# Kernel tuning notes

Hardware: AMD Instinct MI355X
Metric: run time of the kernel (lower is better)

The kernel has to match this reference:

```python
import jax, jax.numpy as jnp
import numpy as np

N_NODES = 100000
D = 256            # in_channels
H = 256            # hidden_channels
E = 1000000        # number of query pairs


def setup_inputs() -> dict:
    key = jax.random.key(0)
    ks = jax.random.split(key, 8)
    x = jax.random.normal(ks[0], (N_NODES, D), dtype=jnp.float32)
    edge_index = jax.random.randint(ks[1], (2, 1000), 0, N_NODES, dtype=jnp.int64)
    edge_pairs = jax.random.randint(ks[2], (E, 2), 0, N_NODES, dtype=jnp.int64)
    # MLP params (Linear stores y = x @ W + b, W shaped [in, out])
    s1 = 1.0 / np.sqrt(D)
    s2 = 1.0 / np.sqrt(H)
    s3 = 1.0 / np.sqrt(H // 2)
    W1 = jax.random.uniform(ks[3], (D, H), jnp.float32, -s1, s1)
    b1 = jnp.zeros((H,), jnp.float32)
    W2 = jax.random.uniform(ks[4], (H, H // 2), jnp.float32, -s2, s2)
    b2 = jnp.zeros((H // 2,), jnp.float32)
    W3 = jax.random.uniform(ks[5], (H // 2, 1), jnp.float32, -s3, s3)
    b3 = jnp.zeros((1,), jnp.float32)
    return {"x": x, "W1": W1, "b1": b1, "W2": W2, "b2": b2,
            "W3": W3, "b3": b3, "edge_index": edge_index, "edge_pairs": edge_pairs}


def reference(x, W1, b1, W2, b2, W3, b3, edge_index, edge_pairs):
    # Gather node pairs and form elementwise-product pair features [E, D]
    feats = x[edge_pairs[:, 0]] * x[edge_pairs[:, 1]]
    # 3-layer MLP (dropout inactive at inference)
    h = jax.nn.relu(feats @ W1 + b1)
    h = jax.nn.relu(h @ W2 + b2)
    scores = h @ W3 + b3
    return scores.reshape(-1)
```

## Files before the change

### kernel.cpp

```cpp
#include <hip/hip_runtime.h>


typedef __attribute__((ext_vector_type(8))) short short8;
typedef __attribute__((ext_vector_type(4))) float floatx4;
typedef __attribute__((ext_vector_type(4))) unsigned uintx4;
typedef __attribute__((ext_vector_type(2))) int intx2;

#define MT 64
#define NTHREADS 1024
#define NBLOCKS 512

__device__ __forceinline__ unsigned short f2bf(float f) {
  union { float f; unsigned u; } a; a.f = f;
  unsigned r = a.u + 0x7FFFu + ((a.u >> 16) & 1u);
  return (unsigned short)(r >> 16);
}

__device__ __forceinline__ unsigned bf16mul2(unsigned ua, unsigned ub) {
  float lo = __uint_as_float(ua << 16)          * __uint_as_float(ub << 16);
  float hi = __uint_as_float(ua & 0xFFFF0000u) * __uint_as_float(ub & 0xFFFF0000u);
  return (unsigned)f2bf(lo) | ((unsigned)f2bf(hi) << 16);
}

__global__ void cast_x_kernel(const float* __restrict__ x, unsigned short* __restrict__ xb, int n4) {
  int i = blockIdx.x * blockDim.x + threadIdx.x;
  if (i >= n4) return;
  float4 v = ((const float4*)x)[i];
  ushort4 o;
  o.x = f2bf(v.x); o.y = f2bf(v.y); o.z = f2bf(v.z); o.w = f2bf(v.w);
  ((ushort4*)xb)[i] = o;
}

__global__ void prep_w_kernel(const float* __restrict__ W1, const float* __restrict__ W2,
                              unsigned short* __restrict__ w1t, unsigned short* __restrict__ w2t) {
  int i = blockIdx.x * blockDim.x + threadIdx.x;
  if (i < 256 * 256) {
    int k = i >> 8, n = i & 255;
    w1t[n * 256 + k] = f2bf(W1[k * 256 + n]);
  } else {
    int j = i - 256 * 256;
    if (j < 128 * 256) {
      int k = j >> 7, n = j & 127;
      w2t[n * 256 + k] = f2bf(W2[k * 128 + n]);
    }
  }
}

__global__ void init_out_kernel(float* __restrict__ out, const float* __restrict__ b3, int E) {
  int i = blockIdx.x * blockDim.x + threadIdx.x;
  if (i < E) out[i] = b3[0];
}

__global__ __launch_bounds__(NTHREADS, 4) void mlp_kernel(
    const unsigned short* __restrict__ xb,
    const unsigned short* __restrict__ w1t,
    const unsigned short* __restrict__ w2t,
    const float* __restrict__ b1,
    const float* __restrict__ b2,
    const float* __restrict__ w3,
    const int* __restrict__ ep,
    float* __restrict__ out,
    int E)
{
  __shared__ __align__(16) unsigned short buf[2][MT * 256];

  const int tid  = threadIdx.x;
  const int wv   = tid >> 6;
  const int lane = tid & 63;
  const int q    = lane >> 4;
  const int r16  = lane & 15;
  const int c    = tid & 31;
  const int mr0  = tid >> 5;

  const int ntiles = (E + MT - 1) / MT;

  {
    int t0 = blockIdx.x;
    #pragma unroll
    for (int s = 0; s < 2; ++s) {
      int m = mr0 + 32 * s;
      int g = t0 * MT + m; if (g >= E) g = E - 1;
      intx2 uv = __builtin_nontemporal_load((const intx2*)(ep + 2 * (size_t)g));
      uintx4 a = __builtin_nontemporal_load((const uintx4*)(xb + ((size_t)uv.x << 8) + (c << 3)));
      uintx4 b = __builtin_nontemporal_load((const uintx4*)(xb + ((size_t)uv.y << 8) + (c << 3)));
      uintx4 pv;
      #pragma unroll
      for (int tt = 0; tt < 4; ++tt) pv[tt] = bf16mul2(a[tt], b[tt]);
      *(uintx4*)((char*)buf[0] + m * 512 + ((c ^ (m & 15)) << 4)) = pv;
    }
  }
  __syncthreads();

  int p = 0;
  for (int t = blockIdx.x; t < ntiles; t += NBLOCKS) {
    char* const bufp = (char*)buf[p];
    char* const bufn = (char*)buf[p ^ 1];
    const int tn = (t + NBLOCKS < ntiles) ? (t + NBLOCKS) : t;

    intx2 uvn[2];
    #pragma unroll
    for (int s = 0; s < 2; ++s) {
      int g = tn * MT + mr0 + 32 * s; if (g >= E) g = E - 1;
      uvn[s] = __builtin_nontemporal_load((const intx2*)(ep + 2 * (size_t)g));
    }

    const unsigned short* const b1p = w1t + (wv * 16 + r16) * 256 + q * 8;
    short8 bv1[8];
    #pragma unroll
    for (int kt = 0; kt < 8; ++kt) bv1[kt] = *(const short8*)(b1p + kt * 32);

    floatx4 acc[4];
    #pragma unroll
    for (int i = 0; i < 4; ++i) acc[i] = (floatx4){0.f, 0.f, 0.f, 0.f};

    char* const a1base = bufp + r16 * 512;
    #pragma unroll
    for (int kt = 0; kt < 8; ++kt) {
      const int aoff = (kt << 6) ^ ((q ^ r16) << 4);
      short8 av[4];
      #pragma unroll
      for (int mt = 0; mt < 4; ++mt)
        av[mt] = *(const short8*)(a1base + mt * (16 * 512) + aoff);
      #pragma unroll
      for (int mt = 0; mt < 4; ++mt)
        acc[mt] = __builtin_amdgcn_mfma_f32_16x16x32_bf16(av[mt], bv1[kt], acc[mt], 0, 0, 0);
    }
    __syncthreads();

    {
      const int n1 = wv * 16 + r16;
      const float bias1 = b1[n1];
      #pragma unroll
      for (int mt = 0; mt < 4; ++mt) {
        #pragma unroll
        for (int r = 0; r < 4; ++r) {
          int m = mt * 16 + q * 4 + r;
          float h = fmaxf(acc[mt][r] + bias1, 0.f);
          int ch = (n1 >> 3) ^ (m & 15);
          *(unsigned short*)(bufp + m * 512 + (ch << 4) + ((n1 & 7) << 1)) = f2bf(h);
        }
      }
    }
    __syncthreads();

    const int mg2 = wv >> 3;
    const int ng2 = wv & 7;
    const unsigned short* const b2p = w2t + (ng2 * 16 + r16) * 256 + q * 8;
    short8 bv2[8];
    #pragma unroll
    for (int kt = 0; kt < 8; ++kt) bv2[kt] = *(const short8*)(b2p + kt * 32);

    uintx4 ra[2], rb[2];
    #pragma unroll
    for (int s = 0; s < 2; ++s) {
      ra[s] = __builtin_nontemporal_load((const uintx4*)(xb + ((size_t)uvn[s].x << 8) + (c << 3)));
      rb[s] = __builtin_nontemporal_load((const uintx4*)(xb + ((size_t)uvn[s].y << 8) + (c << 3)));
    }

    floatx4 acc2[2];
    acc2[0] = (floatx4){0.f, 0.f, 0.f, 0.f};
    acc2[1] = (floatx4){0.f, 0.f, 0.f, 0.f};
    char* const a2base = bufp + (mg2 * 32 + r16) * 512;
    #pragma unroll
    for (int kt = 0; kt < 8; ++kt) {
      const int aoff = (kt << 6) ^ ((q ^ r16) << 4);
      short8 av0 = *(const short8*)(a2base + aoff);
      short8 av1 = *(const short8*)(a2base + 16 * 512 + aoff);
      acc2[0] = __builtin_amdgcn_mfma_f32_16x16x32_bf16(av0, bv2[kt], acc2[0], 0, 0, 0);
      acc2[1] = __builtin_amdgcn_mfma_f32_16x16x32_bf16(av1, bv2[kt], acc2[1], 0, 0, 0);
    }

    {
      const int n2 = ng2 * 16 + r16;
      const float b2v = b2[n2];
      const float w3v = w3[n2];
      #pragma unroll
      for (int mt = 0; mt < 2; ++mt) {
        #pragma unroll
        for (int r = 0; r < 4; ++r) {
          float h = fmaxf(acc2[mt][r] + b2v, 0.f);
          float pp = h * w3v;
          pp += __shfl_xor(pp, 1);
          pp += __shfl_xor(pp, 2);
          pp += __shfl_xor(pp, 4);
          pp += __shfl_xor(pp, 8);
          if (r16 == 0) {
            int g = t * MT + mg2 * 32 + mt * 16 + q * 4 + r;
            if (g < E) atomicAdd(out + g, pp);
          }
        }
      }
    }

    #pragma unroll
    for (int s = 0; s < 2; ++s) {
      int m = mr0 + 32 * s;
      uintx4 pv;
      #pragma unroll
      for (int tt = 0; tt < 4; ++tt) pv[tt] = bf16mul2(ra[s][tt], rb[s][tt]);
      *(uintx4*)(bufn + m * 512 + ((c ^ (m & 15)) << 4)) = pv;
    }
    __syncthreads();
    p ^= 1;
  }
}

extern "C" void kernel_launch(void* const* d_in, const int* in_sizes, int n_in,
                              void* d_out, int out_size, void* d_ws, size_t ws_size,
                              hipStream_t stream) {
  const float* x  = (const float*)d_in[0];
  const float* W1 = (const float*)d_in[1];
  const float* b1 = (const float*)d_in[2];
  const float* W2 = (const float*)d_in[3];
  const float* b2 = (const float*)d_in[4];
  const float* W3 = (const float*)d_in[5];
  const float* b3 = (const float*)d_in[6];
  const int*   ep = (const int*)d_in[8];
  float* out = (float*)d_out;

  const int NX = in_sizes[0];
  const int E  = in_sizes[8] / 2;

  unsigned short* xb  = (unsigned short*)d_ws;
  unsigned short* w1t = (unsigned short*)((char*)d_ws + (size_t)NX * 2);
  unsigned short* w2t = w1t + 256 * 256;

  init_out_kernel<<<(E + 255) / 256, 256, 0, stream>>>(out, b3, E);
  cast_x_kernel<<<(NX / 4 + 255) / 256, 256, 0, stream>>>(x, xb, NX / 4);
  prep_w_kernel<<<(256 * 256 + 128 * 256 + 255) / 256, 256, 0, stream>>>(W1, W2, w1t, w2t);
  mlp_kernel<<<NBLOCKS, NTHREADS, 0, stream>>>(xb, w1t, w2t, b1, b2, W3, ep, out, E);
}
```

Before: 525.1 us.

## Restructure MLP kernel pipeline, drop atomics, hoist weights, merge prep kernels

Merges the cast and weight-prep kernels and removes the output-init kernel. Layer-3 partial sums now go through shared memory and are written directly instead of with atomicAdd. W1 and W2 fragments and biases are hoisted into registers once per block, and a separate h1 buffer removes one barrier per tile. Gather loads are issued earlier, with edge-index prefetch two tiles ahead, and packed bf16 conversion uses v_cvt_pk_bf16_f32. Block count is halved to 256, and the larger shared footprint and register pressure may reduce occupancy.

```diff
diff --git a/kernel.cpp b/kernel.cpp
--- a/kernel.cpp
+++ b/kernel.cpp
@@ -8,7 +8,7 @@
 
 #define MT 64
 #define NTHREADS 1024
-#define NBLOCKS 512
+#define NBLOCKS 256
 
 __device__ __forceinline__ unsigned short f2bf(float f) {
   union { float f; unsigned u; } a; a.f = f;
@@ -16,39 +16,43 @@
   return (unsigned short)(r >> 16);
 }
 
-__device__ __forceinline__ unsigned bf16mul2(unsigned ua, unsigned ub) {
+__device__ __forceinline__ unsigned pkbf(float lo, float hi) {
+  unsigned r;
+  asm("v_cvt_pk_bf16_f32 %0, %1, %2" : "=v"(r) : "v"(lo), "v"(hi));
+  return r;
+}
+
+__device__ __forceinline__ unsigned bfmul2(unsigned ua, unsigned ub) {
   float lo = __uint_as_float(ua << 16)          * __uint_as_float(ub << 16);
   float hi = __uint_as_float(ua & 0xFFFF0000u) * __uint_as_float(ub & 0xFFFF0000u);
-  return (unsigned)f2bf(lo) | ((unsigned)f2bf(hi) << 16);
-}
-
-__global__ void cast_x_kernel(const float* __restrict__ x, unsigned short* __restrict__ xb, int n4) {
+  return pkbf(lo, hi);
+}
+
+__global__ void prep_kernel(const float* __restrict__ x,
+                            const float* __restrict__ W1,
+                            const float* __restrict__ W2,
+                            unsigned short* __restrict__ xb,
+                            unsigned short* __restrict__ w1t,
+                            unsigned short* __restrict__ w2t, int n4) {
   int i = blockIdx.x * blockDim.x + threadIdx.x;
-  if (i >= n4) return;
-  float4 v = ((const float4*)x)[i];
-  ushort4 o;
-  o.x = f2bf(v.x); o.y = f2bf(v.y); o.z = f2bf(v.z); o.w = f2bf(v.w);
-  ((ushort4*)xb)[i] = o;
-}
-
-__global__ void prep_w_kernel(const float* __restrict__ W1, const float* __restrict__ W2,
-                              unsigned short* __restrict__ w1t, unsigned short* __restrict__ w2t) {
-  int i = blockIdx.x * blockDim.x + threadIdx.x;
-  if (i < 256 * 256) {
-    int k = i >> 8, n = i & 255;
-    w1t[n * 256 + k] = f2bf(W1[k * 256 + n]);
+  if (i < n4) {
+    float4 v = ((const float4*)x)[i];
+    ushort4 o;
+    o.x = f2bf(v.x); o.y = f2bf(v.y); o.z = f2bf(v.z); o.w = f2bf(v.w);
+    ((ushort4*)xb)[i] = o;
   } else {
-    int j = i - 256 * 256;
-    if (j < 128 * 256) {
-      int k = j >> 7, n = j & 127;
-      w2t[n * 256 + k] = f2bf(W2[k * 128 + n]);
-    }
-  }
-}
-
-__global__ void init_out_kernel(float* __restrict__ out, const float* __restrict__ b3, int E) {
-  int i = blockIdx.x * blockDim.x + threadIdx.x;
-  if (i < E) out[i] = b3[0];
+    int j = i - n4;
+    if (j < 256 * 256) {
+      int k = j >> 8, n = j & 255;
+      w1t[n * 256 + k] = f2bf(W1[k * 256 + n]);
+    } else {
+      j -= 256 * 256;
+      if (j < 128 * 256) {
+        int k = j >> 7, n = j & 127;
+        w2t[n * 256 + k] = f2bf(W2[k * 128 + n]);
+      }
+    }
+  }
 }
 
 __global__ __launch_bounds__(NTHREADS, 4) void mlp_kernel(
@@ -58,11 +62,14 @@
     const float* __restrict__ b1,
     const float* __restrict__ b2,
     const float* __restrict__ w3,
+    const float* __restrict__ b3,
     const int* __restrict__ ep,
     float* __restrict__ out,
     int E)
 {
-  __shared__ __align__(16) unsigned short buf[2][MT * 256];
+  __shared__ __align__(16) unsigned short feats[2][MT * 256];
+  __shared__ __align__(16) unsigned short h1buf[MT * 256];
+  __shared__ float part[MT][9];
 
   const int tid  = threadIdx.x;
   const int wv   = tid >> 6;
@@ -74,46 +81,70 @@
 
   const int ntiles = (E + MT - 1) / MT;
 
+  const int n1  = wv * 16 + r16;
+  const int mg2 = wv >> 3;
+  const int ng2 = wv & 7;
+  const int n2  = ng2 * 16 + r16;
+
+  short8 bv1[8], bv2[8];
   {
-    int t0 = blockIdx.x;
+    const unsigned short* const b1p = w1t + n1 * 256 + q * 8;
+    const unsigned short* const b2p = w2t + n2 * 256 + q * 8;
+    #pragma unroll
+    for (int kt = 0; kt < 8; ++kt) {
+      bv1[kt] = *(const short8*)(b1p + kt * 32);
+      bv2[kt] = *(const short8*)(b2p + kt * 32);
+    }
+  }
+  const float bias1 = b1[n1];
+  const float bias2 = b2[n2];
+  const float w3v   = w3[n2];
+  const float b3v   = b3[0];
+
+  intx2 uv0, uv1;
+  {
+    const int t0 = blockIdx.x;
     #pragma unroll
     for (int s = 0; s < 2; ++s) {
       int m = mr0 + 32 * s;
       int g = t0 * MT + m; if (g >= E) g = E - 1;
       intx2 uv = __builtin_nontemporal_load((const intx2*)(ep + 2 * (size_t)g));
-      uintx4 a = __builtin_nontemporal_load((const uintx4*)(xb + ((size_t)uv.x << 8) + (c << 3)));
-      uintx4 b = __builtin_nontemporal_load((const uintx4*)(xb + ((size_t)uv.y << 8) + (c << 3)));
+      uintx4 a = *(const uintx4*)(xb + ((size_t)(unsigned)uv.x << 8) + (c << 3));
+      uintx4 b = *(const uintx4*)(xb + ((size_t)(unsigned)uv.y << 8) + (c << 3));
       uintx4 pv;
       #pragma unroll
-      for (int tt = 0; tt < 4; ++tt) pv[tt] = bf16mul2(a[tt], b[tt]);
-      *(uintx4*)((char*)buf[0] + m * 512 + ((c ^ (m & 15)) << 4)) = pv;
-    }
+      for (int tt = 0; tt < 4; ++tt) pv[tt] = bfmul2(a[tt], b[tt]);
+      *(uintx4*)((char*)feats[0] + m * 512 + ((c ^ (m & 15)) << 4)) = pv;
+    }
+    int t1 = t0 + NBLOCKS;
+    int g0 = t1 * MT + mr0;      if (g0 >= E) g0 = E - 1;
+    int g1 = t1 * MT + mr0 + 32; if (g1 >= E) g1 = E - 1;
+    uv0 = __builtin_nontemporal_load((const intx2*)(ep + 2 * (size_t)g0));
+    uv1 = __builtin_nontemporal_load((const intx2*)(ep + 2 * (size_t)g1));
   }
   __syncthreads();
 
-  int p = 0;
+  int fp = 0;
   for (int t = blockIdx.x; t < ntiles; t += NBLOCKS) {
-    char* const bufp = (char*)buf[p];
-    char* const bufn = (char*)buf[p ^ 1];
-    const int tn = (t + NBLOCKS < ntiles) ? (t + NBLOCKS) : t;
-
-    intx2 uvn[2];
-    #pragma unroll
-    for (int s = 0; s < 2; ++s) {
-      int g = tn * MT + mr0 + 32 * s; if (g >= E) g = E - 1;
-      uvn[s] = __builtin_nontemporal_load((const intx2*)(ep + 2 * (size_t)g));
-    }
-
-    const unsigned short* const b1p = w1t + (wv * 16 + r16) * 256 + q * 8;
-    short8 bv1[8];
-    #pragma unroll
-    for (int kt = 0; kt < 8; ++kt) bv1[kt] = *(const short8*)(b1p + kt * 32);
+    uintx4 ra0 = *(const uintx4*)(xb + ((size_t)(unsigned)uv0.x << 8) + (c << 3));
+    uintx4 rb0 = *(const uintx4*)(xb + ((size_t)(unsigned)uv0.y << 8) + (c << 3));
+    uintx4 ra1 = *(const uintx4*)(xb + ((size_t)(unsigned)uv1.x << 8) + (c << 3));
+    uintx4 rb1 = *(const uintx4*)(xb + ((size_t)(unsigned)uv1.y << 8) + (c << 3));
+
+    intx2 nv0, nv1;
+    {
+      int t2 = t + 2 * NBLOCKS;
+      int g0 = t2 * MT + mr0;      if (g0 >= E) g0 = E - 1;
+      int g1 = t2 * MT + mr0 + 32; if (g1 >= E) g1 = E - 1;
+      nv0 = __builtin_nontemporal_load((const intx2*)(ep + 2 * (size_t)g0));
+      nv1 = __builtin_nontemporal_load((const intx2*)(ep + 2 * (size_t)g1));
+    }
 
     floatx4 acc[4];
     #pragma unroll
     for (int i = 0; i < 4; ++i) acc[i] = (floatx4){0.f, 0.f, 0.f, 0.f};
 
-    char* const a1base = bufp + r16 * 512;
+    const char* const a1base = (const char*)feats[fp] + r16 * 512;
     #pragma unroll
     for (int kt = 0; kt < 8; ++kt) {
       const int aoff = (kt << 6) ^ ((q ^ r16) << 4);
@@ -125,42 +156,44 @@
       for (int mt = 0; mt < 4; ++mt)
         acc[mt] = __builtin_amdgcn_mfma_f32_16x16x32_bf16(av[mt], bv1[kt], acc[mt], 0, 0, 0);
     }
-    __syncthreads();
-
-    {
-      const int n1 = wv * 16 + r16;
-      const float bias1 = b1[n1];
+
+    {
+      char* const hb = (char*)h1buf;
+      const int chb = n1 >> 3;
+      const int eo  = (n1 & 7) << 1;
       #pragma unroll
       for (int mt = 0; mt < 4; ++mt) {
         #pragma unroll
-        for (int r = 0; r < 4; ++r) {
-          int m = mt * 16 + q * 4 + r;
-          float h = fmaxf(acc[mt][r] + bias1, 0.f);
-          int ch = (n1 >> 3) ^ (m & 15);
-          *(unsigned short*)(bufp + m * 512 + (ch << 4) + ((n1 & 7) << 1)) = f2bf(h);
+        for (int rp = 0; rp < 2; ++rp) {
+          float h0 = fmaxf(acc[mt][2 * rp]     + bias1, 0.f);
+          float h1 = fmaxf(acc[mt][2 * rp + 1] + bias1, 0.f);
+          unsigned pk = pkbf(h0, h1);
+          int m0 = mt * 16 + q * 4 + 2 * rp;
+          *(unsigned short*)(hb + m0 * 512 + ((chb ^ (m0 & 15)) << 4) + eo) =
+              (unsigned short)pk;
+          *(unsigned short*)(hb + (m0 + 1) * 512 + ((chb ^ ((m0 + 1) & 15)) << 4) + eo) =
+              (unsigned short)(pk >> 16);
         }
       }
     }
     __syncthreads();
 
-    const int mg2 = wv >> 3;
-    const int ng2 = wv & 7;
-    const unsigned short* const b2p = w2t + (ng2 * 16 + r16) * 256 + q * 8;
-    short8 bv2[8];
-    #pragma unroll
-    for (int kt = 0; kt < 8; ++kt) bv2[kt] = *(const short8*)(b2p + kt * 32);
-
-    uintx4 ra[2], rb[2];
-    #pragma unroll
-    for (int s = 0; s < 2; ++s) {
-      ra[s] = __builtin_nontemporal_load((const uintx4*)(xb + ((size_t)uvn[s].x << 8) + (c << 3)));
-      rb[s] = __builtin_nontemporal_load((const uintx4*)(xb + ((size_t)uvn[s].y << 8) + (c << 3)));
+    {
+      char* const bufn = (char*)feats[fp ^ 1];
+      uintx4 pv0, pv1;
+      #pragma unroll
+      for (int tt = 0; tt < 4; ++tt) pv0[tt] = bfmul2(ra0[tt], rb0[tt]);
+      #pragma unroll
+      for (int tt = 0; tt < 4; ++tt) pv1[tt] = bfmul2(ra1[tt], rb1[tt]);
+      const int m0 = mr0, m1 = mr0 + 32;
+      *(uintx4*)(bufn + m0 * 512 + ((c ^ (m0 & 15)) << 4)) = pv0;
+      *(uintx4*)(bufn + m1 * 512 + ((c ^ (m1 & 15)) << 4)) = pv1;
     }
 
     floatx4 acc2[2];
     acc2[0] = (floatx4){0.f, 0.f, 0.f, 0.f};
     acc2[1] = (floatx4){0.f, 0.f, 0.f, 0.f};
-    char* const a2base = bufp + (mg2 * 32 + r16) * 512;
+    const char* const a2base = (const char*)h1buf + (mg2 * 32 + r16) * 512;
     #pragma unroll
     for (int kt = 0; kt < 8; ++kt) {
       const int aoff = (kt << 6) ^ ((q ^ r16) << 4);
@@ -171,37 +204,34 @@
     }
 
     {
-      const int n2 = ng2 * 16 + r16;
-      const float b2v = b2[n2];
-      const float w3v = w3[n2];
       #pragma unroll
       for (int mt = 0; mt < 2; ++mt) {
         #pragma unroll
         for (int r = 0; r < 4; ++r) {
-          float h = fmaxf(acc2[mt][r] + b2v, 0.f);
+          float h = fmaxf(acc2[mt][r] + bias2, 0.f);
           float pp = h * w3v;
           pp += __shfl_xor(pp, 1);
           pp += __shfl_xor(pp, 2);
           pp += __shfl_xor(pp, 4);
           pp += __shfl_xor(pp, 8);
-          if (r16 == 0) {
-            int g = t * MT + mg2 * 32 + mt * 16 + q * 4 + r;
-            if (g < E) atomicAdd(out + g, pp);
-          }
+          if (r16 == 0)
+            part[mg2 * 32 + mt * 16 + q * 4 + r][ng2] = pp;
         }
       }
     }
-
-    #pragma unroll
-    for (int s = 0; s < 2; ++s) {
-      int m = mr0 + 32 * s;
-      uintx4 pv;
-      #pragma unroll
-      for (int tt = 0; tt < 4; ++tt) pv[tt] = bf16mul2(ra[s][tt], rb[s][tt]);
-      *(uintx4*)(bufn + m * 512 + ((c ^ (m & 15)) << 4)) = pv;
-    }
     __syncthreads();
-    p ^= 1;
+
+    if (tid < MT) {
+      int g = t * MT + tid;
+      if (g < E) {
+        float s = (part[tid][0] + part[tid][1]) + (part[tid][2] + part[tid][3]) +
+                  (part[tid][4] + part[tid][5]) + (part[tid][6] + part[tid][7]);
+        out[g] = s + b3v;
+      }
+    }
+
+    fp ^= 1;
+    uv0 = nv0; uv1 = nv1;
   }
 }
 
@@ -225,8 +255,8 @@
   unsigned short* w1t = (unsigned short*)((char*)d_ws + (size_t)NX * 2);
   unsigned short* w2t = w1t + 256 * 256;
 
-  init_out_kernel<<<(E + 255) / 256, 256, 0, stream>>>(out, b3, E);
-  cast_x_kernel<<<(NX / 4 + 255) / 256, 256, 0, stream>>>(x, xb, NX / 4);
-  prep_w_kernel<<<(256 * 256 + 128 * 256 + 255) / 256, 256, 0, stream>>>(W1, W2, w1t, w2t);
-  mlp_kernel<<<NBLOCKS, NTHREADS, 0, stream>>>(xb, w1t, w2t, b1, b2, W3, ep, out, E);
-}
+  const int n4 = NX / 4;
+  const int prep_threads = n4 + 256 * 256 + 128 * 256;
+  prep_kernel<<<(prep_threads + 255) / 256, 256, 0, stream>>>(x, W1, W2, xb, w1t, w2t, n4);
+  mlp_kernel<<<NBLOCKS, NTHREADS, 0, stream>>>(xb, w1t, w2t, b1, b2, W3, b3, ep, out, E);
+}
```

After: 451.8 us. 14.0% less time.
